# Optimization experiments

Measured on AMD Instinct MI355X. Metric: run time of the kernel, lower is better.

Reference implementation:

```python
import jax, jax.numpy as jnp
import numpy as np

B, T, N, F_, KH, D, KD = 16, 12, 325, 64, 4, 16, 3  # batch, time, nodes, feat, heads, head_dim, diffusion steps
H = KH // 2
EPS = 1e-5


def setup_inputs() -> dict:
    key = jax.random.key(0)
    ks = jax.random.split(key, 16)
    lin = lambda k: (jax.random.normal(k, (F_, F_), jnp.float32) * 0.02)
    return {
        "x": jax.random.normal(ks[0], (B, T, N, F_), jnp.float32),
        "A": jax.random.uniform(ks[1], (KD, N, N), jnp.float32),
        "AT": jax.random.uniform(ks[2], (KD, N, N), jnp.float32),
        "Wq": lin(ks[3]), "bq": jnp.zeros((F_,), jnp.float32),
        "Wk": lin(ks[4]), "bk": jnp.zeros((F_,), jnp.float32),
        "Wks": lin(ks[5]), "bks": jnp.zeros((F_,), jnp.float32),
        "Wv": lin(ks[6]), "bv": jnp.zeros((F_,), jnp.float32),
        "Wvs": lin(ks[7]), "bvs": jnp.zeros((F_,), jnp.float32),
        "Wdi": jax.random.normal(ks[8], (H, KD, N, N), jnp.float32) * 0.05,
        "Wdo": jax.random.normal(ks[9], (H, KD, N, N), jnp.float32) * 0.05,
        "Wf1": lin(ks[10]), "bf1": jnp.zeros((F_,), jnp.float32),
        "Wf2": lin(ks[11]), "bf2": jnp.zeros((F_,), jnp.float32),
        "g_ln": jnp.ones((F_,), jnp.float32), "b_ln": jnp.zeros((F_,), jnp.float32),
    }


def _heads(y):
    # [B,T,N,F] -> [KH,B,T,N,D]  (torch.split along -1 then stack on dim 0)
    return y.reshape(B, T, N, KH, D).transpose(3, 0, 1, 2, 4)


def _attn_half(q, k, ks_, v, vs, bias):
    # q,k,ks_,v,vs: [H,B,T,N,D]; bias: [H,1,1,N,N]
    scale = 1.0 / jnp.sqrt(jnp.float32(D))
    e = jnp.einsum('hbtnd,hbtmd->hbtnm', q, k) * scale + bias
    es = jax.nn.sigmoid((q * ks_).sum(-1, keepdims=True) * scale)  # [H,B,T,N,1]
    e = e - e.max(-1, keepdims=True)
    ex = jnp.exp(e)
    a = ex / (es + ex.sum(-1, keepdims=True))  # sigmoid-augmented softmax
    out = jnp.einsum('hbtnm,hbtmd->hbtnd', a, v)
    return out + vs - a.sum(-1, keepdims=True) * vs


def reference(x, A, AT, Wq, bq, Wk, bk, Wks, bks, Wv, bv, Wvs, bvs,
              Wdi, Wdo, Wf1, bf1, Wf2, bf2, g_ln, b_ln):
    q = _heads(x @ Wq.T + bq)
    k = _heads(x @ Wk.T + bk)
    ks_ = _heads(x @ Wks.T + bks)
    v = _heads(x @ Wv.T + bv)
    vs = _heads(x @ Wvs.T + bvs)

    # DCN graph-diffusion bias: sum_j W[h,j] * A[j] -> [H,1,1,N,N]
    bias_i = jnp.einsum('hknm,knm->hnm', Wdi, A)[:, None, None]
    bias_o = jnp.einsum('hknm,knm->hnm', Wdo, AT)[:, None, None]

    vi = _attn_half(q[:H], k[:H], ks_[:H], v[:H], vs[:H], bias_i)
    vo = _attn_half(q[H:], k[H:], ks_[H:], v[H:], vs[H:], bias_o)

    val = jnp.concatenate([vi, vo], 0)  # [KH,B,T,N,D]
    val = val.transpose(1, 2, 3, 0, 4).reshape(B, T, N, F_)

    h = jax.nn.gelu(val @ Wf1.T + bf1, approximate=False) @ Wf2.T + bf2
    h = h + x

    mu = h.mean(-1, keepdims=True)
    var = ((h - mu) ** 2).mean(-1, keepdims=True)
    return g_ln * (h - mu) / jnp.sqrt(var + EPS) + b_ln
```

## Files before the change

kernel.cpp:

```cpp
#include <hip/hip_runtime.h>
#include <hip/hip_bf16.h>
#include <math.h>

#define NN 325
#define FD 64
#define KH 4
#define DH 16
#define BT 192
#define NN2 (NN*NN)
#define PST (NN*DH)
#define VTS  352
#define VSLICE (16*VTS)
#define HSTR 72
#define NPROJ 975
#define NBIAS 1848
#define NPAD  (KH*BT)
#define ANB   4032
#define LOG2E 1.44269504088896f

typedef __attribute__((ext_vector_type(8))) short short8;
typedef __attribute__((ext_vector_type(4))) float f32x4;

union U8 { uint4 u; short8 s; ushort us[8]; };
__device__ inline short8 lds8(const ushort* p){ U8 t; t.u = *(const uint4*)p; return t.s; }
__device__ inline float b2f(ushort v){ return __uint_as_float(((unsigned)v) << 16); }
__device__ inline ushort f2b(float f){
  unsigned u = __float_as_uint(f);
  u += 0x7fff + ((u >> 16) & 1);
  return (ushort)(u >> 16);
}
__device__ inline unsigned pk2(float a, float b){
  union { __hip_bfloat162 h; unsigned u; } t;
  t.h = __float22bfloat162_rn(float2{a, b});
  return t.u;
}
__device__ inline short8 cvt8(const float* p){
  float4 u = ((const float4*)p)[0], v = ((const float4*)p)[1];
  U8 t;
  t.us[0]=f2b(u.x); t.us[1]=f2b(u.y); t.us[2]=f2b(u.z); t.us[3]=f2b(u.w);
  t.us[4]=f2b(v.x); t.us[5]=f2b(v.y); t.us[6]=f2b(v.z); t.us[7]=f2b(v.w);
  return t.s;
}

__global__ __launch_bounds__(256) void wpack_kernel(
    const float* __restrict__ Wq,  const float* __restrict__ bq,
    const float* __restrict__ Wk,  const float* __restrict__ bk,
    const float* __restrict__ Wks, const float* __restrict__ bks,
    const float* __restrict__ Wv,  const float* __restrict__ bv,
    const float* __restrict__ Wvs, const float* __restrict__ bvs,
    const float* __restrict__ Wf1, const float* __restrict__ Wf2,
    ushort* __restrict__ Wcat, float* __restrict__ bcat,
    ushort* __restrict__ idT){
  int blk = blockIdx.x;
  if (blk == 7){
    for (int e = threadIdx.x; e < 672; e += 256){
      int l = e & 31, mm = l & 15, gg = l >> 4;
      U8 t;
      #pragma unroll
      for (int j = 0; j < 8; ++j) t.us[j] = (mm == gg*8 + j) ? (ushort)0x3F80 : (ushort)0;
      *(uint4*)(idT + (size_t)e*8) = t.u;
    }
    return;
  }
  const float* Ws[7] = {Wq, Wk, Wks, Wv, Wvs, Wf1, Wf2};
  const float* bs[5] = {bq, bk, bks, bv, bvs};
  int f = blk * 64 + (threadIdx.x >> 2);
  int c0 = (threadIdx.x & 3) * 8;
  const float* wr = Ws[blk] + (f & 63) * 64;
  unsigned* dst = (unsigned*)Wcat + f * 32 + c0;
  #pragma unroll
  for (int c = 0; c < 8; ++c)
    dst[c] = f2b(wr[2*(c0+c)]) | ((unsigned)f2b(wr[2*(c0+c)+1]) << 16);
  if (blk < 5 && (threadIdx.x & 3) == 0) bcat[f] = bs[blk][f & 63];
}

__global__ __launch_bounds__(256) void prep_kernel(
    const float* __restrict__ x, const ushort* __restrict__ Wcat,
    const float* __restrict__ bcat, ushort* __restrict__ proj,
    ushort* __restrict__ vt,
    const float* __restrict__ Wdi, const float* __restrict__ Wdo,
    const float* __restrict__ A,   const float* __restrict__ AT,
    ushort* __restrict__ biasB){
  int bid = blockIdx.x, tid = threadIdx.x;
  if (bid < NPROJ){
    int lane = tid & 63, wid = tid >> 6;
    int r0 = bid * 64 + wid * 16;
    int m = lane & 15, g = lane >> 4;
    int gr = r0 + m;
    int bt = gr / NN, n = gr - bt * NN;
    const float* xr = x + (size_t)gr * 64 + g * 8;
    short8 xb0 = cvt8(xr);
    short8 xb1 = cvt8(xr + 32);
    for (int ct = 0; ct < 20; ++ct){
      short8 w0 = lds8(Wcat + ((size_t)(ct*16 + m) * 64 + g * 8));
      short8 w1 = lds8(Wcat + ((size_t)(ct*16 + m) * 64 + g * 8 + 32));
      float4 b4 = *(const float4*)(bcat + ct*16 + 4*g);
      f32x4 acc = {b4.x, b4.y, b4.z, b4.w};
      acc = __builtin_amdgcn_mfma_f32_16x16x32_bf16(w0, xb0, acc, 0, 0, 0);
      acc = __builtin_amdgcn_mfma_f32_16x16x32_bf16(w1, xb1, acc, 0, 0, 0);
      if (ct >= 12 && ct < 16){
        ushort* vs = vt + (size_t)((ct-12)*BT + bt) * VSLICE + n;
        #pragma unroll
        for (int rg = 0; rg < 4; ++rg)
          vs[(size_t)(4*g + rg) * VTS] = f2b(acc[rg]);
      } else {
        float sc = (ct < 4) ? 0.25f * LOG2E : 1.0f;
        uint2 w;
        w.x = pk2(acc[0]*sc, acc[1]*sc);
        w.y = pk2(acc[2]*sc, acc[3]*sc);
        *(uint2*)(proj + ((size_t)ct * BT + bt) * PST + n*16 + 4*g) = w;
      }
    }
  } else if (bid < NPROJ + NBIAS){
    int idx = (bid - NPROJ) * 256 + tid;
    int h = idx / 118272;
    int rem = idx - h * 118272;
    int n = rem / 352, mc = rem - n * 352;
    int j = mc >> 4, r = mc & 15;
    int tok = 32*(j>>1) + 8*(r>>2) + 4*(j&1) + (r&3);
    float s = -1e30f;
    if (n < NN && tok < NN){
      int ridx = n * NN + tok;
      s = 0.f;
      if (h < 2){
        #pragma unroll
        for (int k = 0; k < 3; ++k) s += Wdi[(h*3 + k)*NN2 + ridx] * A[k*NN2 + ridx];
      } else {
        int h2 = h - 2;
        #pragma unroll
        for (int k = 0; k < 3; ++k) s += Wdo[(h2*3 + k)*NN2 + ridx] * AT[k*NN2 + ridx];
      }
      s *= LOG2E;
    }
    biasB[idx] = f2b(s);
  } else {
    int slice = bid - NPROJ - NBIAS;
    ushort* vs = vt + (size_t)slice * VSLICE;
    if (tid < 432){
      int d = tid / 27, c = NN + tid % 27;
      vs[(size_t)d * VTS + c] = 0;
    }
  }
}

__global__ __launch_bounds__(256, 4) void attn_kernel(
    const ushort* __restrict__ proj, const ushort* __restrict__ biasB,
    const ushort* __restrict__ idT, const ushort* __restrict__ vt,
    ushort* __restrict__ val){
  int tid = threadIdx.x, lane = tid & 63, wid = tid >> 6;
  int bid = (int)blockIdx.x;
  int swz = (bid & 7) * (ANB/8) + (bid >> 3);
  int tile = swz * 4 + wid;
  int qt = tile % 21, bh = tile / 21;
  int h = bh / BT, bt = bh - h * BT;
  int m = lane & 15, g = lane >> 4;
  int lext = 8*(m >> 2) + (m & 3);

  const ushort* qb  = proj + (size_t)((0*KH + h)*BT + bt) * PST;
  const ushort* kb  = proj + (size_t)((1*KH + h)*BT + bt) * PST;
  const ushort* ksb = proj + (size_t)((2*KH + h)*BT + bt) * PST;
  const ushort* vsb = proj + (size_t)((4*KH + h)*BT + bt) * PST;

  const ushort* vtg = vt + (size_t)(h*BT + bt)*VSLICE + (size_t)m*VTS + g*8;
  short8 vf[11];
  #pragma unroll
  for (int tt = 0; tt < 11; ++tt) vf[tt] = lds8(vtg + tt*32);

  int nq = qt*16 + m, nb = min(nq, NN-1);
  uint2 qw = *(const uint2*)(qb + (size_t)nb*16 + g*4);
  uint2 kw = *(const uint2*)(ksb + (size_t)nb*16 + g*4);

  const ushort* abase = (g < 2) ? (kb + g*8) : (idT + (size_t)(lane & 31)*8);
  int amul = (g < 2) ? 16 : 0;
  const ushort* pbase = (g < 2)
      ? (qb + (size_t)(qt*16 + m)*16 + g*8)
      : (biasB + (size_t)(h*336 + qt*16 + m)*352 + (g-2)*8);
  int bstep = (g < 2) ? 0 : 16;

  short8 aE0 = lds8(abase + min(lext, 324)*amul);
  short8 aO0 = lds8(abase + min(lext + 4, 324)*amul);
  short8 bE0 = lds8(pbase);
  short8 bO0 = lds8(pbase + bstep);

  f32x4 o = {0.f, 0.f, 0.f, 0.f};
  float rowsum = 0.f;
  #pragma unroll
  for (int tt = 0; tt < 11; ++tt){
    short8 aE1 = aE0, aO1 = aO0, bE1 = bE0, bO1 = bO0;
    if (tt < 10){
      int wbase = 32*(tt+1);
      aE1 = lds8(abase + min(wbase + lext,     324)*amul);
      aO1 = lds8(abase + min(wbase + lext + 4, 324)*amul);
      bE1 = lds8(pbase + (2*tt+2)*bstep);
      bO1 = lds8(pbase + (2*tt+3)*bstep);
    }
    f32x4 accE = {0.f,0.f,0.f,0.f}, accO = {0.f,0.f,0.f,0.f};
    accE = __builtin_amdgcn_mfma_f32_16x16x32_bf16(aE0, bE0, accE, 0, 0, 0);
    accO = __builtin_amdgcn_mfma_f32_16x16x32_bf16(aO0, bO0, accO, 0, 0, 0);
    float e0 = __builtin_amdgcn_exp2f(accE[0]);
    float e1 = __builtin_amdgcn_exp2f(accE[1]);
    float e2 = __builtin_amdgcn_exp2f(accE[2]);
    float e3 = __builtin_amdgcn_exp2f(accE[3]);
    float e4 = __builtin_amdgcn_exp2f(accO[0]);
    float e5 = __builtin_amdgcn_exp2f(accO[1]);
    float e6 = __builtin_amdgcn_exp2f(accO[2]);
    float e7 = __builtin_amdgcn_exp2f(accO[3]);
    rowsum += ((e0 + e1) + (e2 + e3)) + ((e4 + e5) + (e6 + e7));
    U8 pf;
    pf.u.x = pk2(e0, e1);
    pf.u.y = pk2(e2, e3);
    pf.u.z = pk2(e4, e5);
    pf.u.w = pk2(e6, e7);
    o = __builtin_amdgcn_mfma_f32_16x16x32_bf16(pf.s, vf[tt], o, 0, 0, 0);
    aE0 = aE1; aO0 = aO1; bE0 = bE1; bO0 = bO1;
  }

  rowsum += __shfl_xor(rowsum, 16, 64);
  rowsum += __shfl_xor(rowsum, 32, 64);

  float dp = b2f((ushort)(qw.x & 0xffff)) * b2f((ushort)(kw.x & 0xffff))
           + b2f((ushort)(qw.x >> 16))    * b2f((ushort)(kw.x >> 16))
           + b2f((ushort)(qw.y & 0xffff)) * b2f((ushort)(kw.y & 0xffff))
           + b2f((ushort)(qw.y >> 16))    * b2f((ushort)(kw.y >> 16));
  dp += __shfl_xor(dp, 16, 64);
  dp += __shfl_xor(dp, 32, 64);
  float esv  = __builtin_amdgcn_rcpf(1.f + __builtin_amdgcn_exp2f(-dp));
  float inv  = __builtin_amdgcn_rcpf(esv + rowsum);
  float beta = 1.f - rowsum * inv;

  int sb = g << 4;
  float invr[4], betr[4];
  #pragma unroll
  for (int rg = 0; rg < 4; ++rg){
    invr[rg] = __uint_as_float(__builtin_amdgcn_ds_bpermute(sb + rg*4, __float_as_uint(inv)));
    betr[rg] = __uint_as_float(__builtin_amdgcn_ds_bpermute(sb + rg*4, __float_as_uint(beta)));
  }
  #pragma unroll
  for (int rg = 0; rg < 4; ++rg){
    int n = qt*16 + 4*g + rg;
    int nc = min(n, NN-1);
    float vsx = b2f(vsb[(size_t)nc*16 + m]);
    float res = o[rg]*invr[rg] + betr[rg]*vsx;
    if (n < NN) val[((size_t)bt*NN + n)*FD + h*16 + m] = f2b(res);
  }
}

__global__ __launch_bounds__(256) void ffn_kernel(
    const ushort* __restrict__ val, const float* __restrict__ x,
    const ushort* __restrict__ Wf1b, const float* __restrict__ bf1,
    const ushort* __restrict__ Wf2b, const float* __restrict__ bf2,
    const float* __restrict__ g_ln, const float* __restrict__ b_ln,
    float* __restrict__ out){
  __shared__ ushort hs[4][16 * HSTR];
  int tid = threadIdx.x, lane = tid & 63, wid = tid >> 6;
  int m = lane & 15, g = lane >> 4;
  int r0 = blockIdx.x * 64 + wid * 16;
  int row = r0 + m;

  short8 vb0 = lds8(val + ((size_t)row * 64 + g * 8));
  short8 vb1 = lds8(val + ((size_t)row * 64 + g * 8 + 32));

  #pragma unroll
  for (int ct = 0; ct < 4; ++ct){
    short8 w0 = lds8(Wf1b + ((size_t)(ct*16 + m) * 64 + g * 8));
    short8 w1 = lds8(Wf1b + ((size_t)(ct*16 + m) * 64 + g * 8 + 32));
    float4 b4 = *(const float4*)(bf1 + ct*16 + 4*g);
    f32x4 acc = {b4.x, b4.y, b4.z, b4.w};
    acc = __builtin_amdgcn_mfma_f32_16x16x32_bf16(w0, vb0, acc, 0, 0, 0);
    acc = __builtin_amdgcn_mfma_f32_16x16x32_bf16(w1, vb1, acc, 0, 0, 0);
    uint2 w;
    float g0 = 0.5f*acc[0]*(1.f + erff(acc[0]*0.70710678118654752f));
    float g1 = 0.5f*acc[1]*(1.f + erff(acc[1]*0.70710678118654752f));
    float g2 = 0.5f*acc[2]*(1.f + erff(acc[2]*0.70710678118654752f));
    float g3 = 0.5f*acc[3]*(1.f + erff(acc[3]*0.70710678118654752f));
    w.x = pk2(g0, g1); w.y = pk2(g2, g3);
    *(uint2*)&hs[wid][m * HSTR + ct*16 + 4*g] = w;
  }
  asm volatile("s_waitcnt lgkmcnt(0)" ::: "memory");
  short8 h0 = lds8(&hs[wid][m * HSTR + g * 8]);
  short8 h1 = lds8(&hs[wid][m * HSTR + g * 8 + 32]);

  float t[4][4];
  #pragma unroll
  for (int ct = 0; ct < 4; ++ct){
    short8 w0 = lds8(Wf2b + ((size_t)(ct*16 + m) * 64 + g * 8));
    short8 w1 = lds8(Wf2b + ((size_t)(ct*16 + m) * 64 + g * 8 + 32));
    float4 b4 = *(const float4*)(bf2 + ct*16 + 4*g);
    f32x4 acc = {b4.x, b4.y, b4.z, b4.w};
    acc = __builtin_amdgcn_mfma_f32_16x16x32_bf16(w0, h0, acc, 0, 0, 0);
    acc = __builtin_amdgcn_mfma_f32_16x16x32_bf16(w1, h1, acc, 0, 0, 0);
    float4 xr = *(const float4*)(x + (size_t)row * 64 + ct*16 + 4*g);
    t[ct][0] = acc[0] + xr.x; t[ct][1] = acc[1] + xr.y;
    t[ct][2] = acc[2] + xr.z; t[ct][3] = acc[3] + xr.w;
  }
  float s = 0.f;
  #pragma unroll
  for (int ct = 0; ct < 4; ++ct) s += (t[ct][0]+t[ct][1]) + (t[ct][2]+t[ct][3]);
  s += __shfl_xor(s, 16, 64); s += __shfl_xor(s, 32, 64);
  float mu = s * (1.f/64.f);
  float v = 0.f;
  #pragma unroll
  for (int ct = 0; ct < 4; ++ct){
    #pragma unroll
    for (int rg = 0; rg < 4; ++rg){ float d = t[ct][rg] - mu; v += d*d; }
  }
  v += __shfl_xor(v, 16, 64); v += __shfl_xor(v, 32, 64);
  float rs = rsqrtf(v * (1.f/64.f) + 1e-5f);
  #pragma unroll
  for (int ct = 0; ct < 4; ++ct){
    float4 g4 = *(const float4*)(g_ln + ct*16 + 4*g);
    float4 bb = *(const float4*)(b_ln + ct*16 + 4*g);
    float4 o;
    o.x = g4.x*(t[ct][0]-mu)*rs + bb.x;
    o.y = g4.y*(t[ct][1]-mu)*rs + bb.y;
    o.z = g4.z*(t[ct][2]-mu)*rs + bb.z;
    o.w = g4.w*(t[ct][3]-mu)*rs + bb.w;
    *(float4*)(out + (size_t)row * 64 + ct*16 + 4*g) = o;
  }
}

extern "C" void kernel_launch(void* const* d_in, const int* in_sizes, int n_in,
                              void* d_out, int out_size, void* d_ws, size_t ws_size,
                              hipStream_t stream) {
  const float* x    = (const float*)d_in[0];
  const float* A    = (const float*)d_in[1];
  const float* AT   = (const float*)d_in[2];
  const float* Wq   = (const float*)d_in[3];
  const float* bq   = (const float*)d_in[4];
  const float* Wk   = (const float*)d_in[5];
  const float* bk   = (const float*)d_in[6];
  const float* Wks  = (const float*)d_in[7];
  const float* bks  = (const float*)d_in[8];
  const float* Wv   = (const float*)d_in[9];
  const float* bv   = (const float*)d_in[10];
  const float* Wvs  = (const float*)d_in[11];
  const float* bvs  = (const float*)d_in[12];
  const float* Wdi  = (const float*)d_in[13];
  const float* Wdo  = (const float*)d_in[14];
  const float* Wf1  = (const float*)d_in[15];
  const float* bf1  = (const float*)d_in[16];
  const float* Wf2  = (const float*)d_in[17];
  const float* bf2  = (const float*)d_in[18];
  const float* g_ln = (const float*)d_in[19];
  const float* b_ln = (const float*)d_in[20];
  float* out = (float*)d_out;

  float* ws = (float*)d_ws;
  ushort* proj  = (ushort*)ws;
  ushort* biasB = (ushort*)(ws + 9984000);
  ushort* idT   = biasB + 473088;
  ushort* val   = (ushort*)(ws + 10441600);
  ushort* vt    = (ushort*)(ws + 12438400);
  ushort* Wcat  = (ushort*)(ws + 14601088);
  float*  bcat  = ws + 14615424;
  ushort* Wf1b  = Wcat + 320*64;
  ushort* Wf2b  = Wcat + 384*64;

  wpack_kernel<<<8, 256, 0, stream>>>(Wq, bq, Wk, bk, Wks, bks,
                                      Wv, bv, Wvs, bvs, Wf1, Wf2, Wcat, bcat, idT);
  prep_kernel<<<NPROJ + NBIAS + NPAD, 256, 0, stream>>>(
      x, Wcat, bcat, proj, vt, Wdi, Wdo, A, AT, biasB);
  attn_kernel<<<ANB, 256, 0, stream>>>(proj, biasB, idT, vt, val);
  ffn_kernel<<<975, 256, 0, stream>>>(val, x, Wf1b, bf1, Wf2b, bf2,
                                      g_ln, b_ln, out);
}
```

Before: 194.8 us.

## Pre-permute K and V into tile layout and add bias after QK MFMA

K and V projections are now written by the prep kernel directly into per-32-token tile layouts (kperm, vt with WSL stride), so the attention kernel loads contiguous 16-byte fragments without min-clamped gathers. The identity-matrix trick that folded the bias into the QK MFMA is dropped. The bias is instead read in a matching tiled layout and added in fp32 before exp2. The V fragments are streamed with a two-deep double buffer instead of preloaded into 11 registers, which lowers register pressure. This adds scalar adds per score and changes the workspace layout and padding-zero logic.

```diff
diff --git a/kernel.cpp b/kernel.cpp
--- a/kernel.cpp
+++ b/kernel.cpp
@@ -9,8 +9,7 @@
 #define BT 192
 #define NN2 (NN*NN)
 #define PST (NN*DH)
-#define VTS  352
-#define VSLICE (16*VTS)
+#define WSL 5632
 #define HSTR 72
 #define NPROJ 975
 #define NBIAS 1848
@@ -49,19 +48,8 @@
     const float* __restrict__ Wv,  const float* __restrict__ bv,
     const float* __restrict__ Wvs, const float* __restrict__ bvs,
     const float* __restrict__ Wf1, const float* __restrict__ Wf2,
-    ushort* __restrict__ Wcat, float* __restrict__ bcat,
-    ushort* __restrict__ idT){
+    ushort* __restrict__ Wcat, float* __restrict__ bcat){
   int blk = blockIdx.x;
-  if (blk == 7){
-    for (int e = threadIdx.x; e < 672; e += 256){
-      int l = e & 31, mm = l & 15, gg = l >> 4;
-      U8 t;
-      #pragma unroll
-      for (int j = 0; j < 8; ++j) t.us[j] = (mm == gg*8 + j) ? (ushort)0x3F80 : (ushort)0;
-      *(uint4*)(idT + (size_t)e*8) = t.u;
-    }
-    return;
-  }
   const float* Ws[7] = {Wq, Wk, Wks, Wv, Wvs, Wf1, Wf2};
   const float* bs[5] = {bq, bk, bks, bv, bvs};
   int f = blk * 64 + (threadIdx.x >> 2);
@@ -77,7 +65,7 @@
 __global__ __launch_bounds__(256) void prep_kernel(
     const float* __restrict__ x, const ushort* __restrict__ Wcat,
     const float* __restrict__ bcat, ushort* __restrict__ proj,
-    ushort* __restrict__ vt,
+    ushort* __restrict__ vt, ushort* __restrict__ kperm,
     const float* __restrict__ Wdi, const float* __restrict__ Wdo,
     const float* __restrict__ A,   const float* __restrict__ AT,
     ushort* __restrict__ biasB){
@@ -98,26 +86,37 @@
       f32x4 acc = {b4.x, b4.y, b4.z, b4.w};
       acc = __builtin_amdgcn_mfma_f32_16x16x32_bf16(w0, xb0, acc, 0, 0, 0);
       acc = __builtin_amdgcn_mfma_f32_16x16x32_bf16(w1, xb1, acc, 0, 0, 0);
-      if (ct >= 12 && ct < 16){
-        ushort* vs = vt + (size_t)((ct-12)*BT + bt) * VSLICE + n;
+      if (ct >= 4 && ct < 8){
+        int w = n & 31;
+        ushort* kd = kperm + (size_t)((ct-4)*BT + bt) * WSL
+                   + (n >> 5)*512 + ((w >> 2) & 1)*256
+                   + (4*(w >> 3) + (w & 3))*16 + 4*g;
+        uint2 wv; wv.x = pk2(acc[0], acc[1]); wv.y = pk2(acc[2], acc[3]);
+        *(uint2*)kd = wv;
+      } else if (ct >= 12 && ct < 16){
+        ushort* vs = vt + (size_t)((ct-12)*BT + bt) * WSL + (n >> 5)*512 + (n & 31);
         #pragma unroll
         for (int rg = 0; rg < 4; ++rg)
-          vs[(size_t)(4*g + rg) * VTS] = f2b(acc[rg]);
+          vs[(4*g + rg) * 32] = f2b(acc[rg]);
       } else {
+        int slot = (ct < 4) ? ct : (ct < 12 ? ct - 4 : ct - 8);
         float sc = (ct < 4) ? 0.25f * LOG2E : 1.0f;
-        uint2 w;
-        w.x = pk2(acc[0]*sc, acc[1]*sc);
-        w.y = pk2(acc[2]*sc, acc[3]*sc);
-        *(uint2*)(proj + ((size_t)ct * BT + bt) * PST + n*16 + 4*g) = w;
+        uint2 w2;
+        w2.x = pk2(acc[0]*sc, acc[1]*sc);
+        w2.y = pk2(acc[2]*sc, acc[3]*sc);
+        *(uint2*)(proj + ((size_t)slot * BT + bt) * PST + n*16 + 4*g) = w2;
       }
     }
   } else if (bid < NPROJ + NBIAS){
     int idx = (bid - NPROJ) * 256 + tid;
     int h = idx / 118272;
     int rem = idx - h * 118272;
-    int n = rem / 352, mc = rem - n * 352;
-    int j = mc >> 4, r = mc & 15;
-    int tok = 32*(j>>1) + 8*(r>>2) + 4*(j&1) + (r&3);
+    int qt = rem / 5632;
+    int r2 = rem - qt * 5632;
+    int tt = r2 >> 9, r3 = r2 & 511;
+    int mq = r3 >> 5, w = r3 & 31;
+    int n = qt*16 + mq;
+    int tok = tt*32 + w;
     float s = -1e30f;
     if (n < NN && tok < NN){
       int ridx = n * NN + tok;
@@ -135,17 +134,18 @@
     biasB[idx] = f2b(s);
   } else {
     int slice = bid - NPROJ - NBIAS;
-    ushort* vs = vt + (size_t)slice * VSLICE;
     if (tid < 432){
-      int d = tid / 27, c = NN + tid % 27;
-      vs[(size_t)d * VTS + c] = 0;
+      int d = tid / 27, wz = 5 + tid % 27;
+      vt[(size_t)slice * WSL + 5120 + d*32 + wz] = 0;
+      int half = (wz >> 2) & 1, rr = 4*(wz >> 3) + (wz & 3);
+      kperm[(size_t)slice * WSL + 5120 + half*256 + rr*16 + d] = 0;
     }
   }
 }
 
 __global__ __launch_bounds__(256, 4) void attn_kernel(
     const ushort* __restrict__ proj, const ushort* __restrict__ biasB,
-    const ushort* __restrict__ idT, const ushort* __restrict__ vt,
+    const ushort* __restrict__ vt, const ushort* __restrict__ kperm,
     ushort* __restrict__ val){
   int tid = threadIdx.x, lane = tid & 63, wid = tid >> 6;
   int bid = (int)blockIdx.x;
@@ -154,65 +154,62 @@
   int qt = tile % 21, bh = tile / 21;
   int h = bh / BT, bt = bh - h * BT;
   int m = lane & 15, g = lane >> 4;
-  int lext = 8*(m >> 2) + (m & 3);
 
   const ushort* qb  = proj + (size_t)((0*KH + h)*BT + bt) * PST;
-  const ushort* kb  = proj + (size_t)((1*KH + h)*BT + bt) * PST;
-  const ushort* ksb = proj + (size_t)((2*KH + h)*BT + bt) * PST;
-  const ushort* vsb = proj + (size_t)((4*KH + h)*BT + bt) * PST;
-
-  const ushort* vtg = vt + (size_t)(h*BT + bt)*VSLICE + (size_t)m*VTS + g*8;
-  short8 vf[11];
-  #pragma unroll
-  for (int tt = 0; tt < 11; ++tt) vf[tt] = lds8(vtg + tt*32);
+  const ushort* ksb = proj + (size_t)((1*KH + h)*BT + bt) * PST;
+  const ushort* vsb = proj + (size_t)((2*KH + h)*BT + bt) * PST;
+  const ushort* kpb = kperm + (size_t)(h*BT + bt) * WSL;
+  const ushort* vtb = vt    + (size_t)(h*BT + bt) * WSL;
+  const ushort* bbb = biasB + (size_t)(h*21 + qt) * WSL;
+
+  short8 zero = {0,0,0,0,0,0,0,0};
+  short8 qf = (g < 2) ? lds8(qb + (size_t)(qt*16 + m)*16 + (g&1)*8) : zero;
+
+  const ushort* ka = kpb + m*16 + (g&1)*8;
+  const ushort* ba = bbb + m*32 + g*8;
+  const ushort* va = vtb + m*32 + g*8;
 
   int nq = qt*16 + m, nb = min(nq, NN-1);
   uint2 qw = *(const uint2*)(qb + (size_t)nb*16 + g*4);
   uint2 kw = *(const uint2*)(ksb + (size_t)nb*16 + g*4);
 
-  const ushort* abase = (g < 2) ? (kb + g*8) : (idT + (size_t)(lane & 31)*8);
-  int amul = (g < 2) ? 16 : 0;
-  const ushort* pbase = (g < 2)
-      ? (qb + (size_t)(qt*16 + m)*16 + g*8)
-      : (biasB + (size_t)(h*336 + qt*16 + m)*352 + (g-2)*8);
-  int bstep = (g < 2) ? 0 : 16;
-
-  short8 aE0 = lds8(abase + min(lext, 324)*amul);
-  short8 aO0 = lds8(abase + min(lext + 4, 324)*amul);
-  short8 bE0 = lds8(pbase);
-  short8 bO0 = lds8(pbase + bstep);
+  short8 aE[2], aO[2], bf[2], vf[2];
+  aE[0] = lds8(ka);       aO[0] = lds8(ka + 256);
+  bf[0] = lds8(ba);       vf[0] = lds8(va);
+  aE[1] = lds8(ka + 512); aO[1] = lds8(ka + 768);
+  bf[1] = lds8(ba + 512); vf[1] = lds8(va + 512);
 
   f32x4 o = {0.f, 0.f, 0.f, 0.f};
   float rowsum = 0.f;
   #pragma unroll
   for (int tt = 0; tt < 11; ++tt){
-    short8 aE1 = aE0, aO1 = aO0, bE1 = bE0, bO1 = bO0;
-    if (tt < 10){
-      int wbase = 32*(tt+1);
-      aE1 = lds8(abase + min(wbase + lext,     324)*amul);
-      aO1 = lds8(abase + min(wbase + lext + 4, 324)*amul);
-      bE1 = lds8(pbase + (2*tt+2)*bstep);
-      bO1 = lds8(pbase + (2*tt+3)*bstep);
+    const int cur = tt & 1;
+    short8 aEc = aE[cur], aOc = aO[cur], bfc = bf[cur], vfc = vf[cur];
+    if (tt + 2 < 11){
+      aE[cur] = lds8(ka + (tt+2)*512);
+      aO[cur] = lds8(ka + (tt+2)*512 + 256);
+      bf[cur] = lds8(ba + (tt+2)*512);
+      vf[cur] = lds8(va + (tt+2)*512);
     }
     f32x4 accE = {0.f,0.f,0.f,0.f}, accO = {0.f,0.f,0.f,0.f};
-    accE = __builtin_amdgcn_mfma_f32_16x16x32_bf16(aE0, bE0, accE, 0, 0, 0);
-    accO = __builtin_amdgcn_mfma_f32_16x16x32_bf16(aO0, bO0, accO, 0, 0, 0);
-    float e0 = __builtin_amdgcn_exp2f(accE[0]);
-    float e1 = __builtin_amdgcn_exp2f(accE[1]);
-    float e2 = __builtin_amdgcn_exp2f(accE[2]);
-    float e3 = __builtin_amdgcn_exp2f(accE[3]);
-    float e4 = __builtin_amdgcn_exp2f(accO[0]);
-    float e5 = __builtin_amdgcn_exp2f(accO[1]);
-    float e6 = __builtin_amdgcn_exp2f(accO[2]);
-    float e7 = __builtin_amdgcn_exp2f(accO[3]);
+    accE = __builtin_amdgcn_mfma_f32_16x16x32_bf16(aEc, qf, accE, 0, 0, 0);
+    accO = __builtin_amdgcn_mfma_f32_16x16x32_bf16(aOc, qf, accO, 0, 0, 0);
+    U8 bu; bu.s = bfc;
+    float e0 = __builtin_amdgcn_exp2f(accE[0] + b2f(bu.us[0]));
+    float e1 = __builtin_amdgcn_exp2f(accE[1] + b2f(bu.us[1]));
+    float e2 = __builtin_amdgcn_exp2f(accE[2] + b2f(bu.us[2]));
+    float e3 = __builtin_amdgcn_exp2f(accE[3] + b2f(bu.us[3]));
+    float e4 = __builtin_amdgcn_exp2f(accO[0] + b2f(bu.us[4]));
+    float e5 = __builtin_amdgcn_exp2f(accO[1] + b2f(bu.us[5]));
+    float e6 = __builtin_amdgcn_exp2f(accO[2] + b2f(bu.us[6]));
+    float e7 = __builtin_amdgcn_exp2f(accO[3] + b2f(bu.us[7]));
     rowsum += ((e0 + e1) + (e2 + e3)) + ((e4 + e5) + (e6 + e7));
     U8 pf;
     pf.u.x = pk2(e0, e1);
     pf.u.y = pk2(e2, e3);
     pf.u.z = pk2(e4, e5);
     pf.u.w = pk2(e6, e7);
-    o = __builtin_amdgcn_mfma_f32_16x16x32_bf16(pf.s, vf[tt], o, 0, 0, 0);
-    aE0 = aE1; aO0 = aO1; bE0 = bE1; bO0 = bO1;
+    o = __builtin_amdgcn_mfma_f32_16x16x32_bf16(pf.s, vfc, o, 0, 0, 0);
   }
 
   rowsum += __shfl_xor(rowsum, 16, 64);
@@ -347,20 +344,20 @@
 
   float* ws = (float*)d_ws;
   ushort* proj  = (ushort*)ws;
-  ushort* biasB = (ushort*)(ws + 9984000);
-  ushort* idT   = biasB + 473088;
-  ushort* val   = (ushort*)(ws + 10441600);
-  ushort* vt    = (ushort*)(ws + 12438400);
-  ushort* Wcat  = (ushort*)(ws + 14601088);
-  float*  bcat  = ws + 14615424;
+  ushort* biasB = (ushort*)(ws + 5990400);
+  ushort* val   = (ushort*)(ws + 6226944);
+  ushort* vt    = (ushort*)(ws + 8223744);
+  ushort* kperm = (ushort*)(ws + 10386432);
+  ushort* Wcat  = (ushort*)(ws + 12549120);
+  float*  bcat  = ws + 12563456;
   ushort* Wf1b  = Wcat + 320*64;
   ushort* Wf2b  = Wcat + 384*64;
 
-  wpack_kernel<<<8, 256, 0, stream>>>(Wq, bq, Wk, bk, Wks, bks,
-                                      Wv, bv, Wvs, bvs, Wf1, Wf2, Wcat, bcat, idT);
+  wpack_kernel<<<7, 256, 0, stream>>>(Wq, bq, Wk, bk, Wks, bks,
+                                      Wv, bv, Wvs, bvs, Wf1, Wf2, Wcat, bcat);
   prep_kernel<<<NPROJ + NBIAS + NPAD, 256, 0, stream>>>(
-      x, Wcat, bcat, proj, vt, Wdi, Wdo, A, AT, biasB);
-  attn_kernel<<<ANB, 256, 0, stream>>>(proj, biasB, idT, vt, val);
+      x, Wcat, bcat, proj, vt, kperm, Wdi, Wdo, A, AT, biasB);
+  attn_kernel<<<ANB, 256, 0, stream>>>(proj, biasB, vt, kperm, val);
   ffn_kernel<<<975, 256, 0, stream>>>(val, x, Wf1b, bf1, Wf2b, bf2,
                                       g_ln, b_ln, out);
 }
```

New measurement: 190.0 us. 1.03x faster.
